# Performance work log

Hardware: AMD Instinct MI355X
Metric: run time of the kernel (lower is better)

Reference implementation:

```python
import jax, jax.numpy as jnp
import numpy as np

N_NODES = 400
HID = 96
DEC = 64
FEAT_STATIC = 8
FEAT = FEAT_STATIC + N_NODES  # 408
EPS = 1e-8


def prelu(x, a):
    # single-parameter PReLU (torch default num_parameters=1)
    return jnp.where(x >= 0, x, a * x)


def setup_inputs() -> dict:
    key = jax.random.key(0)
    ks = jax.random.split(key, 16)
    B = 16
    E = N_NODES * (N_NODES - 1) // 2  # 79800

    x = jax.random.normal(ks[0], (B, E), dtype=jnp.float32)
    node_features = jax.random.normal(ks[1], (B, N_NODES, FEAT_STATIC), dtype=jnp.float32)
    sc_matrix = jax.random.uniform(ks[2], (B, N_NODES, N_NODES), dtype=jnp.float32)

    # normalization buffers (computed from train split in torch; random stand-ins)
    static_mean = jax.random.normal(ks[3], (1, 1, FEAT_STATIC), dtype=jnp.float32) * 0.1
    static_std = jnp.ones((1, 1, FEAT_STATIC), dtype=jnp.float32)

    def lin(k, fin, fout):
        kw, kb = jax.random.split(k)
        lim = 1.0 / np.sqrt(fin)
        W = jax.random.uniform(kw, (fin, fout), minval=-lim, maxval=lim, dtype=jnp.float32)
        b = jax.random.uniform(kb, (fout,), minval=-lim, maxval=lim, dtype=jnp.float32)
        return W, b

    W_e1, b_e1 = lin(ks[4], FEAT, HID)
    W_e2, b_e2 = lin(ks[5], HID, HID)
    W_d1, b_d1 = lin(ks[6], 3 * HID, DEC)  # symmetric decoder: 3 * node_embed_dim
    W_d2, b_d2 = lin(ks[7], DEC, DEC)
    W_d3, b_d3 = lin(ks[8], DEC, 1)

    a25 = jnp.float32(0.25)

    ei_np, ej_np = np.triu_indices(N_NODES, k=1)
    ei = jnp.asarray(ei_np, dtype=jnp.int32)
    ej = jnp.asarray(ej_np, dtype=jnp.int32)

    return {
        "x": x, "node_features": node_features, "sc_matrix": sc_matrix,
        "static_mean": static_mean, "static_std": static_std,
        "W_e1": W_e1, "b_e1": b_e1, "a_e1": a25,
        "W_e2": W_e2, "b_e2": b_e2, "a_e2": a25,
        "W_d1": W_d1, "b_d1": b_d1, "a_d1": a25,
        "W_d2": W_d2, "b_d2": b_d2, "a_d2": a25,
        "W_d3": W_d3, "b_d3": b_d3,
        "ei": ei, "ej": ej,
    }


def reference(x, node_features, sc_matrix, static_mean, static_std,
              W_e1, b_e1, a_e1, W_e2, b_e2, a_e2,
              W_d1, b_d1, a_d1, W_d2, b_d2, a_d2, W_d3, b_d3, ei, ej):
    # x (SC upper triangle) is only used for batch size in the torch module.
    # static anatomical block: z-score with train stats
    s = (node_features - static_mean) / (static_std + EPS)  # [B,N,8]
    # sc_row block, 'brain_scale': divide by per-matrix mean
    m = sc_matrix / jnp.maximum(
        jnp.mean(sc_matrix, axis=(-2, -1), keepdims=True), EPS)  # [B,N,N]
    feats = jnp.concatenate([s, m], axis=-1)  # [B,N,408]

    # shared node encoder (dropout inactive at eval)
    h = prelu(feats @ W_e1 + b_e1, a_e1)
    h = prelu(h @ W_e2 + b_e2, a_e2)  # [B,N,96]

    # per-edge gather over upper-triangle indices
    h_i = h[:, ei, :]  # [B,E,96]
    h_j = h[:, ej, :]
    # symmetric edge features
    edge_feat = jnp.concatenate(
        [h_i + h_j, jnp.abs(h_i - h_j), h_i * h_j], axis=-1)  # [B,E,288]

    z = prelu(edge_feat @ W_d1 + b_d1, a_d1)
    z = prelu(z @ W_d2 + b_d2, a_d2)
    out = (z @ W_d3 + b_d3)[..., 0]  # [B,E]
    return out
```

## Files before the change

### kernel.cpp

```cpp
#include <hip/hip_runtime.h>

#define NN 400
#define HID 96
#define EDGES 79800
#define BATCH 16
#define ROWS (BATCH*EDGES)
#define NT 13
#define NPAIRS 91

typedef _Float16 f16;
typedef f16 f16x2 __attribute__((ext_vector_type(2)));
typedef f16 f16x8 __attribute__((ext_vector_type(8)));
typedef __fp16 fp16x2 __attribute__((ext_vector_type(2)));
typedef float f32x16 __attribute__((ext_vector_type(16)));
typedef unsigned int u32;
typedef unsigned long long u64;

union H8 { f16x8 h; u32 u[4]; f16x2 p[4]; fp16x2 q[4]; u64 d[2]; };
union C2 { f16x2 h; fp16x2 q; u32 u; };

__device__ inline f16x2 pkrtz(float a, float b) {
  C2 c; c.q = __builtin_amdgcn_cvt_pkrtz(a, b); return c.h;
}
__device__ inline u32 pkrtz_u(float a, float b) {
  C2 c; c.q = __builtin_amdgcn_cvt_pkrtz(a, b); return c.u;
}
__device__ inline float fdot2a(f16x2 a, f16x2 b, float c) {
#if __has_builtin(__builtin_amdgcn_fdot2)
  C2 ca, cb; ca.h = a; cb.h = b;
  return __builtin_amdgcn_fdot2(ca.q, cb.q, c, false);
#else
  return c + (float)a.x*(float)b.x + (float)a.y*(float)b.y;
#endif
}

__device__ inline f16x8 habs8(f16x8 x) {
  H8 t; t.h = x;
  t.u[0] &= 0x7fff7fffu; t.u[1] &= 0x7fff7fffu;
  t.u[2] &= 0x7fff7fffu; t.u[3] &= 0x7fff7fffu;
  return t.h;
}

__device__ inline f16x8 pack8(float a0,float a1,float a2,float a3,
                              float a4,float a5,float a6,float a7){
  H8 u;
  u.p[0] = pkrtz(a0,a1);
  u.p[1] = pkrtz(a2,a3);
  u.p[2] = pkrtz(a4,a5);
  u.p[3] = pkrtz(a6,a7);
  return u.h;
}

__device__ inline void plswap(u32 &x, u32 &y) {
  auto r = __builtin_amdgcn_permlane32_swap((int)x, (int)y, false, false);
  x = (u32)r[0]; y = (u32)r[1];
}

#define MEMFENCE asm volatile("" ::: "memory")

__global__ void prep_mean_kernel(const float* __restrict__ We1, const float* __restrict__ We2,
                                 const float* __restrict__ W1, const float* __restrict__ W2,
                                 const float* __restrict__ sc,
                                 u32* __restrict__ wq, float* __restrict__ mpart) {
  if (blockIdx.x >= 140) {
    int p = blockIdx.x - 140;
    int b = p >> 4, part = p & 15;
    const float4* src = (const float4*)(sc + (size_t)b*160000) + part*2500;
    float s = 0.f;
    for (int i = threadIdx.x; i < 2500; i += 256) {
      float4 v = src[i];
      s += (v.x + v.y) + (v.z + v.w);
    }
    __shared__ float red[256];
    red[threadIdx.x] = s; __syncthreads();
    for (int off = 128; off > 0; off >>= 1) {
      if (threadIdx.x < off) red[threadIdx.x] += red[threadIdx.x + off];
      __syncthreads();
    }
    if (threadIdx.x == 0) mpart[p] = red[0];
    return;
  }
  int D = blockIdx.x*256 + threadIdx.x;
  float v0, v1;
  if (D < 9216) {
    int frag = D >> 8;  int t = frag >> 1, q = frag & 1;
    int rem = D & 255;  int lane = rem >> 2, dj = rem & 3;
    int c = lane & 31, h2 = lane >> 5;
    int k = 16*t + 8*h2 + 2*dj;
    int d = 32*q + c;
    v0 = W1[k*64 + d]; v1 = W1[(k+1)*64 + d];
  } else if (D < 11264) {
    int Dl = D - 9216;
    int frag = Dl >> 8; int t2 = frag >> 1, q = frag & 1;
    int rem = Dl & 255; int lane = rem >> 2, dj = rem & 3;
    int c = lane & 31, h2 = lane >> 5;
    int k = 16*t2 + 8*h2 + 2*dj;
    int d = 32*q + c;
    v0 = W2[k*64 + d]; v1 = W2[(k+1)*64 + d];
  } else if (D < 31232) {
    int Dl = D - 11264;
    int frag = Dl >> 8; int t = frag/3, ct = frag - 3*t;
    int rem = Dl & 255; int lane = rem >> 2, dj = rem & 3;
    int c = lane & 31, h2 = lane >> 5;
    int k0 = 16*t + 8*h2 + 2*dj, k1 = k0 + 1;
    int d = 32*ct + c;
    v0 = (k0 < 400) ? We1[(8+k0)*96 + d] : (k0 < 408 ? We1[(k0-400)*96 + d] : 0.f);
    v1 = (k1 < 400) ? We1[(8+k1)*96 + d] : (k1 < 408 ? We1[(k1-400)*96 + d] : 0.f);
  } else {
    int Dl = D - 31232;
    int frag = Dl >> 8; int t = frag/3, ct = frag - 3*t;
    int rem = Dl & 255; int lane = rem >> 2, dj = rem & 3;
    int c = lane & 31, h2 = lane >> 5;
    int k = 16*t + 8*h2 + 2*dj;
    int d = 32*ct + c;
    v0 = We2[k*96 + d]; v1 = We2[(k+1)*96 + d];
  }
  wq[D] = pkrtz_u(v0, v1);
}

__global__ __launch_bounds__(256) void enc_kernel(
    const float* __restrict__ sc, const float* __restrict__ nf,
    const float* __restrict__ smean, const float* __restrict__ sstd,
    const float* __restrict__ be1, const float* __restrict__ ae1,
    const float* __restrict__ be2, const float* __restrict__ ae2,
    const float* __restrict__ mpart, const u32* __restrict__ wq,
    f16* __restrict__ hout) {
  __shared__ u32 lds[6720 + 1600];
  const int tid = threadIdx.x;
  const int wid = tid >> 6, lane = tid & 63;
  const int c = lane & 31, h2 = lane >> 5;
  const int r0 = blockIdx.x * 32;
  {
    int row = tid >> 3, seg = tid & 7;
    int r = r0 + row;
    int b = r / 400;
    float ms = 0.f;
    const float4* mp4 = (const float4*)(mpart + 16*b);
#pragma unroll
    for (int k = 0; k < 4; ++k) { float4 v = mp4[k]; ms += (v.x+v.y)+(v.z+v.w); }
    float rm = 1.f / fmaxf(ms*(1.f/160000.f), 1e-8f);
    const float4* src = (const float4*)(sc + (size_t)r*400);
#pragma unroll
    for (int i = 0; i < 13; ++i) {
      int col4 = seg + 8*i;
      if (col4 < 100) {
        float4 v = src[col4];
        u32 lo = pkrtz_u(v.x*rm, v.y*rm);
        u32 hi = pkrtz_u(v.z*rm, v.w*rm);
        *(u64*)(lds + row*210 + col4*2) = (u64)lo | ((u64)hi << 32);
      }
    }
  }
  f16x8 bfr[26], we2r[6], af25;
  if (wid < 3) {
    const u32* wb1 = wq + 11264;
#pragma unroll
    for (int t = 0; t < 26; ++t)
      bfr[t] = *(const f16x8*)(wb1 + ((t*3+wid)*64 + lane)*4);
    const u32* wb2 = wq + 31232;
#pragma unroll
    for (int t = 0; t < 6; ++t)
      we2r[t] = *(const f16x8*)(wb2 + ((t*3+wid)*64 + lane)*4);
    af25 = (f16x8){};
    if (h2 == 0) {
      int r = r0 + c;
      float q0[8];
#pragma unroll
      for (int j = 0; j < 8; ++j)
        q0[j] = (nf[r*8 + j] - smean[j]) / (sstd[j] + 1e-8f);
      af25 = pack8(q0[0],q0[1],q0[2],q0[3],q0[4],q0[5],q0[6],q0[7]);
    }
  }
  __syncthreads();
  f16* zb16 = (f16*)(lds + 6720);
  if (wid < 3) {
    const float a1 = *ae1;
    float bv = be1[32*wid + c];
    f32x16 acc;
#pragma unroll
    for (int i = 0; i < 16; ++i) acc[i] = bv;
#pragma unroll
    for (int t = 0; t < 25; ++t) {
      H8 av;
      const u32* ap = lds + c*210 + 8*t + 4*h2;
      av.d[0] = *(const u64*)ap;
      av.d[1] = *(const u64*)(ap + 2);
      acc = __builtin_amdgcn_mfma_f32_32x32x16_f16(av.h, bfr[t], acc, 0,0,0);
    }
    acc = __builtin_amdgcn_mfma_f32_32x32x16_f16(af25, bfr[25], acc, 0,0,0);
#pragma unroll
    for (int r = 0; r < 16; ++r) {
      float v = acc[r]; v = fmaxf(v, a1*v);
      int row = (r & 3) + 8*(r >> 2) + 4*h2;
      zb16[row*100 + 32*wid + c] = (f16)v;
    }
  }
  __syncthreads();
  if (wid < 3) {
    const float a2 = *ae2;
    float bv = be2[32*wid + c];
    f32x16 acc2;
#pragma unroll
    for (int i = 0; i < 16; ++i) acc2[i] = bv;
#pragma unroll
    for (int t = 0; t < 6; ++t) {
      f16x8 af = *(const f16x8*)(zb16 + c*100 + 16*t + 8*h2);
      acc2 = __builtin_amdgcn_mfma_f32_32x32x16_f16(af, we2r[t], acc2, 0,0,0);
    }
#pragma unroll
    for (int rr = 0; rr < 16; ++rr) {
      int row = (rr & 3) + 8*(rr >> 2) + 4*h2;
      float v = acc2[rr]; v = fmaxf(v, a2*v);
      hout[(r0 + row)*96 + 32*wid + c] = (f16)v;
    }
  }
}

__global__ __launch_bounds__(256, 3) void decoder_kernel(
    const f16* __restrict__ hbuf, const u32* __restrict__ wq,
    const float* __restrict__ b1, const float* __restrict__ b2,
    const float* __restrict__ ad1, const float* __restrict__ ad2,
    const float* __restrict__ W3, const float* __restrict__ b3p,
    float* __restrict__ out) {
  __shared__ alignas(16) u32 smem[12960];
  const int tid = threadIdx.x;
  int p = blockIdx.x;
  int b = p / NPAIRS, pr = p - b*NPAIRS;
  int I = 0;
  while (pr >= NT - I) { pr -= NT - I; ++I; }
  const int J = I + pr;
  for (int i = tid; i < 384; i += 256) {
    int row = i / 12, off = i - row*12;
    int nb = I*32 + row; nb = nb < NN ? nb : NN-1;
    const float4* src = (const float4*)(hbuf + (size_t)(b*NN + nb)*HID) + off;
    *((float4*)(smem + row*48) + off) = *src;
  }
  {
    float4* dst = (float4*)(smem + 1536);
    const float4* srcw = (const float4*)wq;
    for (int i = tid; i < 2816; i += 256) dst[i] = srcw[i];
  }
  if (tid < 64) {
    ((float*)(smem + 12800))[tid] = b1[tid];
    ((float*)(smem + 12864))[tid] = b2[tid];
  }
  if (tid < 32) {
    int hh = tid >> 4, rem = tid & 15, q2 = rem >> 3, a = rem & 7;
    int base = 32*q2 + 8*(a >> 1) + 2*(a & 1) + 4*hh;
    smem[12928 + tid] = pkrtz_u(W3[base], W3[base + 1]);
  }

  const int lane = tid & 63;
  const int wid  = tid >> 6;
  const int c = lane & 31, h2 = lane >> 5;
  const int gj = J*32 + c;
  const int gjc = gj < NN ? gj : NN-1;
  f16x8 hjr[6];
  {
    const f16* hjp = hbuf + (size_t)(b*NN + gjc)*HID + 8*h2;
#pragma unroll
    for (int t = 0; t < 6; ++t) hjr[t] = *(const f16x8*)(hjp + 16*t);
  }
  const float a1 = *ad1, a2 = *ad2, b3 = *b3p;
  const f16x2 a1v = pkrtz(a1, a1);
  const f16x2 a2v = pkrtz(a2, a2);
  __syncthreads();

  const f16* hIb = (const f16*)smem;
  const u32* wfr = smem + 1536;
  const u32* w2a = smem + 10752;
  const float* b1f = (const float*)(smem + 12800);
  const float* b2f = (const float*)(smem + 12864);
  const u32* w3l = smem + 12928;
  const int bofs = b*EDGES;

#pragma unroll 1
  for (int it = 0; it < 4; ++it) {
    MEMFENCE;
    const int i0 = it*8 + wid*2;
    const f16* hi0 = hIb + (i0+0)*HID;
    const f16* hi1 = hIb + (i0+1)*HID;
    f32x16 acc[2][2];
#pragma unroll
    for (int q = 0; q < 2; ++q)
#pragma unroll
      for (int a = 0; a < 8; ++a) {
        int base = 32*q + 8*(a >> 1) + 2*(a & 1) + 4*h2;
        float2 bv = *(const float2*)(b1f + base);
        acc[0][q][2*a] = bv.x; acc[0][q][2*a+1] = bv.y;
        acc[1][q][2*a] = bv.x; acc[1][q][2*a+1] = bv.y;
      }
#pragma unroll
    for (int t = 0; t < 6; ++t) {
      MEMFENCE;
      f16x8 as0 = *(const f16x8*)(wfr + (((t    )*2+0)*64 + lane)*4);
      f16x8 as1 = *(const f16x8*)(wfr + (((t    )*2+1)*64 + lane)*4);
      f16x8 ad0 = *(const f16x8*)(wfr + (((t+ 6)*2+0)*64 + lane)*4);
      f16x8 ad1_ = *(const f16x8*)(wfr + (((t+ 6)*2+1)*64 + lane)*4);
      f16x8 ap0 = *(const f16x8*)(wfr + (((t+12)*2+0)*64 + lane)*4);
      f16x8 ap1 = *(const f16x8*)(wfr + (((t+12)*2+1)*64 + lane)*4);
      f16x8 hj8 = hjr[t];
#pragma unroll
      for (int m = 0; m < 2; ++m) {
        f16x8 hi8 = *(const f16x8*)((m ? hi1 : hi0) + 16*t + 8*h2);
        f16x8 su = hi8 + hj8;
        f16x8 di = habs8(hi8 - hj8);
        f16x8 prd = hi8 * hj8;
        __builtin_amdgcn_s_setprio(1);
        acc[m][0] = __builtin_amdgcn_mfma_f32_32x32x16_f16(as0, su,  acc[m][0], 0,0,0);
        acc[m][1] = __builtin_amdgcn_mfma_f32_32x32x16_f16(as1, su,  acc[m][1], 0,0,0);
        acc[m][0] = __builtin_amdgcn_mfma_f32_32x32x16_f16(ad0, di,  acc[m][0], 0,0,0);
        acc[m][1] = __builtin_amdgcn_mfma_f32_32x32x16_f16(ad1_, di, acc[m][1], 0,0,0);
        acc[m][0] = __builtin_amdgcn_mfma_f32_32x32x16_f16(ap0, prd, acc[m][0], 0,0,0);
        acc[m][1] = __builtin_amdgcn_mfma_f32_32x32x16_f16(ap1, prd, acc[m][1], 0,0,0);
        __builtin_amdgcn_s_setprio(0);
      }
    }
#pragma unroll
    for (int m = 0; m < 2; ++m) {
      MEMFENCE;
      u32 w[16];
#pragma unroll
      for (int q = 0; q < 2; ++q)
#pragma unroll
        for (int a = 0; a < 8; ++a) {
          f16x2 pz = pkrtz(acc[m][q][2*a], acc[m][q][2*a+1]);
          pz = __builtin_elementwise_max(pz, pz * a1v);
          C2 cv; cv.h = pz; w[q*8 + a] = cv.u;
        }
#pragma unroll
      for (int g = 0; g < 4; ++g) {
        plswap(w[g*4+0], w[g*4+2]);
        plswap(w[g*4+1], w[g*4+3]);
      }
      f32x16 zacc[2];
#pragma unroll
      for (int q = 0; q < 2; ++q)
#pragma unroll
        for (int a = 0; a < 8; ++a) {
          int base = 32*q + 8*(a >> 1) + 2*(a & 1) + 4*h2;
          float2 bv = *(const float2*)(b2f + base);
          zacc[q][2*a] = bv.x; zacc[q][2*a+1] = bv.y;
        }
#pragma unroll
      for (int t2 = 0; t2 < 4; ++t2) {
        MEMFENCE;
        H8 zf; zf.u[0] = w[4*t2]; zf.u[1] = w[4*t2+1]; zf.u[2] = w[4*t2+2]; zf.u[3] = w[4*t2+3];
        f16x8 w20 = *(const f16x8*)(w2a + ((t2*2+0)*64 + lane)*4);
        f16x8 w21 = *(const f16x8*)(w2a + ((t2*2+1)*64 + lane)*4);
        __builtin_amdgcn_s_setprio(1);
        zacc[0] = __builtin_amdgcn_mfma_f32_32x32x16_f16(w20, zf.h, zacc[0], 0,0,0);
        zacc[1] = __builtin_amdgcn_mfma_f32_32x32x16_f16(w21, zf.h, zacc[1], 0,0,0);
        __builtin_amdgcn_s_setprio(0);
      }
      float s0 = 0.f, s1 = 0.f;
#pragma unroll
      for (int a = 0; a < 8; ++a) {
        C2 wv0; wv0.u = w3l[(h2 << 4) | a];
        f16x2 pz0 = pkrtz(zacc[0][2*a], zacc[0][2*a+1]);
        pz0 = __builtin_elementwise_max(pz0, pz0 * a2v);
        s0 = fdot2a(pz0, wv0.h, s0);
        C2 wv1; wv1.u = w3l[(h2 << 4) | 8 | a];
        f16x2 pz1 = pkrtz(zacc[1][2*a], zacc[1][2*a+1]);
        pz1 = __builtin_elementwise_max(pz1, pz1 * a2v);
        s1 = fdot2a(pz1, wv1.h, s1);
      }
      float ssum = s0 + s1;
      ssum += __shfl_xor(ssum, 32);
      int gi = I*32 + i0 + m;
      if (h2 == 0 && gi < gj && gj < NN) {
        int eo = bofs + gi*(799 - gi)/2 + (gj - gi - 1);
        out[eo] = ssum + b3;
      }
    }
  }
}

extern "C" void kernel_launch(void* const* d_in, const int* in_sizes, int n_in,
                              void* d_out, int out_size, void* d_ws, size_t ws_size,
                              hipStream_t stream) {
  const float* nf  = (const float*)d_in[1];
  const float* sc  = (const float*)d_in[2];
  const float* sm  = (const float*)d_in[3];
  const float* ss  = (const float*)d_in[4];
  const float* We1 = (const float*)d_in[5];
  const float* be1 = (const float*)d_in[6];
  const float* ae1 = (const float*)d_in[7];
  const float* We2 = (const float*)d_in[8];
  const float* be2 = (const float*)d_in[9];
  const float* ae2 = (const float*)d_in[10];
  const float* W1  = (const float*)d_in[11];
  const float* b1  = (const float*)d_in[12];
  const float* a1  = (const float*)d_in[13];
  const float* W2  = (const float*)d_in[14];
  const float* b2  = (const float*)d_in[15];
  const float* a2  = (const float*)d_in[16];
  const float* W3  = (const float*)d_in[17];
  const float* b3  = (const float*)d_in[18];
  float* out = (float*)d_out;

  char* ws = (char*)d_ws;
  float* mpart = (float*)ws;
  f16*   hbuf = (f16*)(ws + 1024);
  u32*   wq   = (u32*)(ws + 1024 + 1228800);

  prep_mean_kernel<<<396, 256, 0, stream>>>(We1, We2, W1, W2, sc, wq, mpart);
  enc_kernel<<<200, 256, 0, stream>>>(sc, nf, sm, ss, be1, ae1, be2, ae2,
                                      mpart, wq, hbuf);
  decoder_kernel<<<BATCH*NPAIRS, 256, 0, stream>>>(hbuf, wq, b1, b2, a1, a2,
                                                   W3, b3, out);
}
```

Before: 178.6 us.

## Precompute per-node projection of sum term to drop it from edge decoder

Uses linearity: (h_i+h_j)·W_sum = h_i·W_sum + h_j·W_sum. The encoder now computes a per-node 64-wide projection u = h·W_sum with MFMA and writes it to a workspace buffer. The decoder seeds its first-layer accumulators with bias plus u_i plus u_j and drops the sum block, cutting its first-layer MFMAs by a third and shrinking the LDS weight copy. In exchange the encoder does extra work and writes an fp32 buffer, the decoder reads more per-node data, and the u terms are added in fp32 instead of going through the fp16 product.

After: 170.0 us. 4.8% less time.

```diff
diff --git a/kernel.cpp b/kernel.cpp
--- a/kernel.cpp
+++ b/kernel.cpp
@@ -124,8 +124,8 @@
     const float* __restrict__ be1, const float* __restrict__ ae1,
     const float* __restrict__ be2, const float* __restrict__ ae2,
     const float* __restrict__ mpart, const u32* __restrict__ wq,
-    f16* __restrict__ hout) {
-  __shared__ u32 lds[6720 + 1600];
+    f16* __restrict__ hout, float* __restrict__ ubuf) {
+  __shared__ u32 lds[6720 + 1600 + 1600];
   const int tid = threadIdx.x;
   const int wid = tid >> 6, lane = tid & 63;
   const int c = lane & 31, h2 = lane >> 5;
@@ -151,7 +151,7 @@
       }
     }
   }
-  f16x8 bfr[26], we2r[6], af25;
+  f16x8 bfr[26], we2r[6], af25, wsf[6];
   if (wid < 3) {
     const u32* wb1 = wq + 11264;
 #pragma unroll
@@ -171,6 +171,11 @@
       af25 = pack8(q0[0],q0[1],q0[2],q0[3],q0[4],q0[5],q0[6],q0[7]);
     }
   }
+  if (wid < 2) {
+#pragma unroll
+    for (int t = 0; t < 6; ++t)
+      wsf[t] = *(const f16x8*)(wq + ((t*2+wid)*64 + lane)*4);
+  }
   __syncthreads();
   f16* zb16 = (f16*)(lds + 6720);
   if (wid < 3) {
@@ -196,6 +201,7 @@
     }
   }
   __syncthreads();
+  f16* hl = (f16*)(lds + 6720 + 1600);
   if (wid < 3) {
     const float a2 = *ae2;
     float bv = be2[32*wid + c];
@@ -211,8 +217,24 @@
     for (int rr = 0; rr < 16; ++rr) {
       int row = (rr & 3) + 8*(rr >> 2) + 4*h2;
       float v = acc2[rr]; v = fmaxf(v, a2*v);
-      hout[(r0 + row)*96 + 32*wid + c] = (f16)v;
-    }
+      f16 hv = (f16)v;
+      hout[(r0 + row)*96 + 32*wid + c] = hv;
+      hl[row*100 + 32*wid + c] = hv;
+    }
+  }
+  __syncthreads();
+  if (wid < 2) {
+    f32x16 au = {};
+#pragma unroll
+    for (int t = 0; t < 6; ++t) {
+      f16x8 hf = *(const f16x8*)(hl + c*100 + 16*t + 8*h2);
+      au = __builtin_amdgcn_mfma_f32_32x32x16_f16(wsf[t], hf, au, 0,0,0);
+    }
+    float* up = ubuf + (size_t)(r0 + c)*64 + h2*32 + wid*16;
+    union { f32x16 v; float4 f[4]; } uu; uu.v = au;
+#pragma unroll
+    for (int i4 = 0; i4 < 4; ++i4)
+      *(float4*)(up + 4*i4) = uu.f[i4];
   }
 }
 
@@ -221,8 +243,8 @@
     const float* __restrict__ b1, const float* __restrict__ b2,
     const float* __restrict__ ad1, const float* __restrict__ ad2,
     const float* __restrict__ W3, const float* __restrict__ b3p,
-    float* __restrict__ out) {
-  __shared__ alignas(16) u32 smem[12960];
+    const float* __restrict__ ubuf, float* __restrict__ out) {
+  __shared__ alignas(16) u32 smem[11936];
   const int tid = threadIdx.x;
   int p = blockIdx.x;
   int b = p / NPAIRS, pr = p - b*NPAIRS;
@@ -237,17 +259,26 @@
   }
   {
     float4* dst = (float4*)(smem + 1536);
-    const float4* srcw = (const float4*)wq;
-    for (int i = tid; i < 2816; i += 256) dst[i] = srcw[i];
+    const float4* srcw = (const float4*)wq + 768;
+    for (int i = tid; i < 2048; i += 256) dst[i] = srcw[i];
+  }
+  {
+    const float4* us = (const float4*)(ubuf + (size_t)(b*NN)*64);
+    float4* ud = (float4*)(smem + 9888);
+    for (int i = tid; i < 512; i += 256) {
+      int row = i >> 4, off = i & 15;
+      int nb = I*32 + row; nb = nb < NN ? nb : NN-1;
+      ud[row*16 + off] = us[nb*16 + off];
+    }
   }
   if (tid < 64) {
-    ((float*)(smem + 12800))[tid] = b1[tid];
-    ((float*)(smem + 12864))[tid] = b2[tid];
+    ((float*)(smem + 9728))[tid] = b1[tid];
+    ((float*)(smem + 9792))[tid] = b2[tid];
   }
   if (tid < 32) {
     int hh = tid >> 4, rem = tid & 15, q2 = rem >> 3, a = rem & 7;
     int base = 32*q2 + 8*(a >> 1) + 2*(a & 1) + 4*hh;
-    smem[12928 + tid] = pkrtz_u(W3[base], W3[base + 1]);
+    smem[9856 + tid] = pkrtz_u(W3[base], W3[base + 1]);
   }
 
   const int lane = tid & 63;
@@ -261,6 +292,12 @@
 #pragma unroll
     for (int t = 0; t < 6; ++t) hjr[t] = *(const f16x8*)(hjp + 16*t);
   }
+  union { float4 f4[8]; float s[32]; } u_j;
+  {
+    const float4* ujp = (const float4*)(ubuf + (size_t)(b*NN + gjc)*64 + h2*32);
+#pragma unroll
+    for (int i4 = 0; i4 < 8; ++i4) u_j.f4[i4] = ujp[i4];
+  }
   const float a1 = *ad1, a2 = *ad2, b3 = *b3p;
   const f16x2 a1v = pkrtz(a1, a1);
   const f16x2 a2v = pkrtz(a2, a2);
@@ -268,10 +305,11 @@
 
   const f16* hIb = (const f16*)smem;
   const u32* wfr = smem + 1536;
-  const u32* w2a = smem + 10752;
-  const float* b1f = (const float*)(smem + 12800);
-  const float* b2f = (const float*)(smem + 12864);
-  const u32* w3l = smem + 12928;
+  const u32* w2a = smem + 7680;
+  const float* b1f = (const float*)(smem + 9728);
+  const float* b2f = (const float*)(smem + 9792);
+  const u32* w3l = smem + 9856;
+  const float* uIf = (const float*)(smem + 9888);
   const int bofs = b*EDGES;
 
 #pragma unroll 1
@@ -280,6 +318,8 @@
     const int i0 = it*8 + wid*2;
     const f16* hi0 = hIb + (i0+0)*HID;
     const f16* hi1 = hIb + (i0+1)*HID;
+    const float* uI0 = uIf + (i0+0)*64 + h2*32;
+    const float* uI1 = uIf + (i0+1)*64 + h2*32;
     f32x16 acc[2][2];
 #pragma unroll
     for (int q = 0; q < 2; ++q)
@@ -287,28 +327,28 @@
       for (int a = 0; a < 8; ++a) {
         int base = 32*q + 8*(a >> 1) + 2*(a & 1) + 4*h2;
         float2 bv = *(const float2*)(b1f + base);
-        acc[0][q][2*a] = bv.x; acc[0][q][2*a+1] = bv.y;
-        acc[1][q][2*a] = bv.x; acc[1][q][2*a+1] = bv.y;
+        float2 ui0 = *(const float2*)(uI0 + q*16 + 2*a);
+        float2 ui1 = *(const float2*)(uI1 + q*16 + 2*a);
+        float uj0 = u_j.s[q*16 + 2*a], uj1 = u_j.s[q*16 + 2*a + 1];
+        acc[0][q][2*a]   = bv.x + ui0.x + uj0;
+        acc[0][q][2*a+1] = bv.y + ui0.y + uj1;
+        acc[1][q][2*a]   = bv.x + ui1.x + uj0;
+        acc[1][q][2*a+1] = bv.y + ui1.y + uj1;
       }
 #pragma unroll
     for (int t = 0; t < 6; ++t) {
       MEMFENCE;
-      f16x8 as0 = *(const f16x8*)(wfr + (((t    )*2+0)*64 + lane)*4);
-      f16x8 as1 = *(const f16x8*)(wfr + (((t    )*2+1)*64 + lane)*4);
-      f16x8 ad0 = *(const f16x8*)(wfr + (((t+ 6)*2+0)*64 + lane)*4);
-      f16x8 ad1_ = *(const f16x8*)(wfr + (((t+ 6)*2+1)*64 + lane)*4);
-      f16x8 ap0 = *(const f16x8*)(wfr + (((t+12)*2+0)*64 + lane)*4);
-      f16x8 ap1 = *(const f16x8*)(wfr + (((t+12)*2+1)*64 + lane)*4);
+      f16x8 ad0 = *(const f16x8*)(wfr + (((t  )*2+0)*64 + lane)*4);
+      f16x8 ad1_ = *(const f16x8*)(wfr + (((t  )*2+1)*64 + lane)*4);
+      f16x8 ap0 = *(const f16x8*)(wfr + (((t+6)*2+0)*64 + lane)*4);
+      f16x8 ap1 = *(const f16x8*)(wfr + (((t+6)*2+1)*64 + lane)*4);
       f16x8 hj8 = hjr[t];
 #pragma unroll
       for (int m = 0; m < 2; ++m) {
         f16x8 hi8 = *(const f16x8*)((m ? hi1 : hi0) + 16*t + 8*h2);
-        f16x8 su = hi8 + hj8;
         f16x8 di = habs8(hi8 - hj8);
         f16x8 prd = hi8 * hj8;
         __builtin_amdgcn_s_setprio(1);
-        acc[m][0] = __builtin_amdgcn_mfma_f32_32x32x16_f16(as0, su,  acc[m][0], 0,0,0);
-        acc[m][1] = __builtin_amdgcn_mfma_f32_32x32x16_f16(as1, su,  acc[m][1], 0,0,0);
         acc[m][0] = __builtin_amdgcn_mfma_f32_32x32x16_f16(ad0, di,  acc[m][0], 0,0,0);
         acc[m][1] = __builtin_amdgcn_mfma_f32_32x32x16_f16(ad1_, di, acc[m][1], 0,0,0);
         acc[m][0] = __builtin_amdgcn_mfma_f32_32x32x16_f16(ap0, prd, acc[m][0], 0,0,0);
@@ -403,10 +443,11 @@
   float* mpart = (float*)ws;
   f16*   hbuf = (f16*)(ws + 1024);
   u32*   wq   = (u32*)(ws + 1024 + 1228800);
+  float* ubuf = (float*)(ws + 1024 + 1228800 + 143360);
 
   prep_mean_kernel<<<396, 256, 0, stream>>>(We1, We2, W1, W2, sc, wq, mpart);
   enc_kernel<<<200, 256, 0, stream>>>(sc, nf, sm, ss, be1, ae1, be2, ae2,
-                                      mpart, wq, hbuf);
+                                      mpart, wq, hbuf, ubuf);
   decoder_kernel<<<BATCH*NPAIRS, 256, 0, stream>>>(hbuf, wq, b1, b2, a1, a2,
-                                                   W3, b3, out);
-}
+                                                   W3, b3, ubuf, out);
+}
```
